# Performance work log

Hardware: AMD Instinct MI355X
Metric: run time of the kernel (lower is better)

## Reference

```python
import jax, jax.numpy as jnp
import numpy as np

N_STREAMS = 4
TAU = 1.0
ALPHA = 0.1
CAYLEY_ITERS = 2
LN_EPS = 1e-5


def setup_inputs() -> dict:
    key = jax.random.key(0)
    k1, k2, k3 = jax.random.split(key, 3)
    b, l, d = 2, 4096, 2048
    n = N_STREAMS
    x = jax.random.normal(k1, (b, l, d), dtype=jnp.float32)
    ln_w = jnp.ones((d,), dtype=jnp.float32)
    ln_b = jnp.zeros((d,), dtype=jnp.float32)
    # CastedLinear: trunc_normal std = 1/sqrt(in_features)
    proj_w = jax.random.truncated_normal(k2, -2.0, 2.0, (3 * n * n, d), dtype=jnp.float32) / jnp.sqrt(d * 1.0)
    proj_b = jnp.zeros((3 * n * n,), dtype=jnp.float32)
    # sublayer_fn realized as a dense linear (typical transformer sublayer core)
    W_sub = jax.random.normal(k3, (d, d), dtype=jnp.float32) / jnp.sqrt(d * 1.0)
    return {"x": x, "ln_w": ln_w, "ln_b": ln_b, "proj_w": proj_w, "proj_b": proj_b, "W_sub": W_sub}


def _layernorm(x, w, b):
    mu = jnp.mean(x, axis=-1, keepdims=True)
    var = jnp.mean(jnp.square(x - mu), axis=-1, keepdims=True)
    return (x - mu) * jax.lax.rsqrt(var + LN_EPS) * w + b


def _iterative_cayley(raw):
    # raw: (b, l, n, n) fp32
    w = raw - jnp.swapaxes(raw, -1, -2)
    eye = jnp.eye(N_STREAMS, dtype=raw.dtype)
    y = eye + ALPHA * w
    for _ in range(CAYLEY_ITERS):
        y = eye + 0.5 * ALPHA * jnp.matmul(w, eye + y)
    return y


def reference(x, ln_w, ln_b, proj_w, proj_b, W_sub):
    b, l, d = x.shape
    n = N_STREAMS
    gates = _layernorm(x, ln_w, ln_b) @ proj_w.T + proj_b  # (b, l, 3*n*n)
    pre_raw, post_raw, res_raw = jnp.split(gates, 3, axis=-1)
    pre_raw = pre_raw.reshape(b, l, n, n).astype(jnp.float32)
    post_raw = post_raw.reshape(b, l, n, n).astype(jnp.float32)
    res_raw = res_raw.reshape(b, l, n, n).astype(jnp.float32)
    h_pre = jax.nn.softmax(pre_raw / TAU, axis=-1)
    h_post = jax.nn.softmax(post_raw / TAU, axis=-2)
    h_res = _iterative_cayley(res_raw)
    # All streams of x_streams are identical copies of x, so
    # einsum('blij,bljd->blid', h, x_streams).mean(-2) == mean_i(sum_j h[i,j]) * x.
    coeff_pre = jnp.mean(jnp.sum(h_pre, axis=-1), axis=-1)    # (b, l)
    coeff_res = jnp.mean(jnp.sum(h_res, axis=-1), axis=-1)    # (b, l)
    coeff_post = jnp.mean(jnp.sum(h_post, axis=-1), axis=-1)  # (b, l)
    x_in = coeff_pre[..., None] * x
    y = x_in @ W_sub  # sublayer_fn
    return coeff_res[..., None] * x + coeff_post[..., None] * y
```

## Files before the change

### kernel.cpp

```cpp
#include <hip/hip_runtime.h>
#include <stdint.h>


typedef __attribute__((ext_vector_type(8))) __bf16 bf16x8;
typedef __attribute__((ext_vector_type(4))) float f32x4;
typedef __attribute__((ext_vector_type(8))) unsigned short us8;
typedef __attribute__((ext_vector_type(4))) unsigned short us4;

__device__ __forceinline__ unsigned short f2bf(float f) {
  union { float f; unsigned int u; } v; v.f = f;
  unsigned int u = v.u;
  u += 0x7fffu + ((u >> 16) & 1u);
  return (unsigned short)(u >> 16);
}

__device__ __forceinline__ void gload_lds16(const void* g, void* l) {
  __builtin_amdgcn_global_load_lds(
      (__attribute__((address_space(1))) void*)g,
      (__attribute__((address_space(3))) void*)l, 16, 0, 0);
}

__global__ __launch_bounds__(256) void k_ln_conv(
    const float* __restrict__ x, const float* __restrict__ lw, const float* __restrict__ lb,
    unsigned short* __restrict__ xb, unsigned short* __restrict__ lnb, int D) {
  const int t = blockIdx.x;
  const int tid = threadIdx.x;
  const float* row = x + (size_t)t * D;
  f32x4 a = *(const f32x4*)(row + tid * 8);
  f32x4 b = *(const f32x4*)(row + tid * 8 + 4);
  float vv[8] = {a[0], a[1], a[2], a[3], b[0], b[1], b[2], b[3]};
  float s = 0.f, ss = 0.f;
#pragma unroll
  for (int j = 0; j < 8; ++j) { s += vv[j]; ss += vv[j] * vv[j]; }
#pragma unroll
  for (int off = 32; off > 0; off >>= 1) { s += __shfl_down(s, off); ss += __shfl_down(ss, off); }
  __shared__ float red[8];
  __shared__ float st[2];
  int lane = tid & 63, wv = tid >> 6;
  if (lane == 0) { red[wv] = s; red[4 + wv] = ss; }
  __syncthreads();
  if (tid == 0) {
    float S = red[0] + red[1] + red[2] + red[3];
    float SS = red[4] + red[5] + red[6] + red[7];
    float mu = S / (float)D;
    float var = SS / (float)D - mu * mu;
    st[0] = mu; st[1] = rsqrtf(var + 1e-5f);
  }
  __syncthreads();
  float mu = st[0], rstd = st[1];
  f32x4 w0 = *(const f32x4*)(lw + tid * 8), w1 = *(const f32x4*)(lw + tid * 8 + 4);
  f32x4 b0 = *(const f32x4*)(lb + tid * 8), b1 = *(const f32x4*)(lb + tid * 8 + 4);
  float ww[8] = {w0[0], w0[1], w0[2], w0[3], w1[0], w1[1], w1[2], w1[3]};
  float bb[8] = {b0[0], b0[1], b0[2], b0[3], b1[0], b1[1], b1[2], b1[3]};
  us8 ox, ol;
#pragma unroll
  for (int j = 0; j < 8; ++j) {
    ox[j] = f2bf(vv[j]);
    ol[j] = f2bf((vv[j] - mu) * rstd * ww[j] + bb[j]);
  }
  *(us8*)(xb + (size_t)t * D + tid * 8) = ox;
  *(us8*)(lnb + (size_t)t * D + tid * 8) = ol;
}

__global__ __launch_bounds__(256) void k_wt(const float* __restrict__ W,
                                            unsigned short* __restrict__ Wt, int D) {
  __shared__ float tile[64][65];
  int kb = blockIdx.x * 64, nb = blockIdx.y * 64;
  int tid = threadIdx.x;
  int tx = tid & 15, ty = tid >> 4;
#pragma unroll
  for (int p = 0; p < 4; ++p) {
    int r = p * 16 + ty;
    f32x4 v = *(const f32x4*)(W + (size_t)(kb + r) * D + nb + tx * 4);
    tile[r][tx * 4 + 0] = v[0]; tile[r][tx * 4 + 1] = v[1];
    tile[r][tx * 4 + 2] = v[2]; tile[r][tx * 4 + 3] = v[3];
  }
  __syncthreads();
#pragma unroll
  for (int p = 0; p < 2; ++p) {
    int c = p * 256 + tid;
    int nr = c >> 3, kc = (c & 7) * 8;
    us8 o;
#pragma unroll
    for (int j = 0; j < 8; ++j) o[j] = f2bf(tile[kc + j][nr]);
    *(us8*)(Wt + (size_t)(nb + nr) * D + kb + kc) = o;
  }
}

__global__ void k_pconv(const float* __restrict__ p, unsigned short* __restrict__ q, int n) {
  int i = (blockIdx.x * 256 + threadIdx.x) * 4;
  if (i < n) {
    f32x4 v = *(const f32x4*)(p + i);
    us4 o;
#pragma unroll
    for (int j = 0; j < 4; ++j) o[j] = f2bf(v[j]);
    *(us4*)(q + i) = o;
  }
}

__global__ __launch_bounds__(256) void k_gates(
    const unsigned short* __restrict__ A,
    const unsigned short* __restrict__ Bp,
    const float* __restrict__ pb,
    float* __restrict__ cresp, float* __restrict__ cpyp, int K) {
  __shared__ __attribute__((aligned(16))) unsigned short As[128 * 32];
  __shared__ __attribute__((aligned(16))) unsigned short Bs[48 * 32];
  __shared__ float gl[128][49];
  __shared__ float pbs[48];
  int tid = threadIdx.x, lane = tid & 63, wv = tid >> 6;
  if (tid < 48) pbs[tid] = pb[tid];
  f32x4 acc[2][3] = {};
  size_t rowBase = (size_t)blockIdx.x * 128;
  for (int k0 = 0; k0 < K; k0 += 32) {
#pragma unroll
    for (int inst = 0; inst < 2; ++inst) {
      int eo = inst * 2048 + wv * 512 + lane * 8;
      int r = eo >> 5, cc = eo & 31;
      gload_lds16(A + (rowBase + r) * K + k0 + cc, (char*)As + inst * 4096 + wv * 1024);
    }
    if (tid < 192) {
      int r = tid >> 2, cc = (tid & 3) * 8;
      us8 v = *(const us8*)(Bp + (size_t)r * K + k0 + cc);
      *(us8*)(Bs + r * 32 + cc) = v;
    }
    __syncthreads();
    int kb = (lane >> 4) * 8, rr = lane & 15;
    bf16x8 av[2], bv[3];
#pragma unroll
    for (int mi = 0; mi < 2; ++mi)
      av[mi] = *(const bf16x8*)(As + (wv * 32 + mi * 16 + rr) * 32 + kb);
#pragma unroll
    for (int ni = 0; ni < 3; ++ni)
      bv[ni] = *(const bf16x8*)(Bs + (ni * 16 + rr) * 32 + kb);
#pragma unroll
    for (int mi = 0; mi < 2; ++mi)
#pragma unroll
      for (int ni = 0; ni < 3; ++ni)
        acc[mi][ni] = __builtin_amdgcn_mfma_f32_16x16x32_bf16(av[mi], bv[ni], acc[mi][ni], 0, 0, 0);
    __syncthreads();
  }
#pragma unroll
  for (int mi = 0; mi < 2; ++mi)
#pragma unroll
    for (int ni = 0; ni < 3; ++ni)
#pragma unroll
      for (int i = 0; i < 4; ++i)
        gl[wv * 32 + mi * 16 + (lane >> 4) * 4 + i][ni * 16 + (lane & 15)] = acc[mi][ni][i];
  __syncthreads();
  if (tid < 128) {
    float g[48];
#pragma unroll
    for (int j = 0; j < 48; ++j) g[j] = gl[tid][j] + pbs[j];
    float cpre = 0.f;
#pragma unroll
    for (int i = 0; i < 4; ++i) {
      float m = fmaxf(fmaxf(g[i * 4], g[i * 4 + 1]), fmaxf(g[i * 4 + 2], g[i * 4 + 3]));
      float e0 = expf(g[i * 4] - m), e1 = expf(g[i * 4 + 1] - m);
      float e2 = expf(g[i * 4 + 2] - m), e3 = expf(g[i * 4 + 3] - m);
      float inv = 1.f / (e0 + e1 + e2 + e3);
      cpre += e0 * inv + e1 * inv + e2 * inv + e3 * inv;
    }
    cpre *= 0.25f;
    float cpost = 0.f;
#pragma unroll
    for (int j = 0; j < 4; ++j) {
      float a0 = g[16 + j], a1 = g[20 + j], a2 = g[24 + j], a3 = g[28 + j];
      float m = fmaxf(fmaxf(a0, a1), fmaxf(a2, a3));
      float e0 = expf(a0 - m), e1 = expf(a1 - m), e2 = expf(a2 - m), e3 = expf(a3 - m);
      float inv = 1.f / (e0 + e1 + e2 + e3);
      cpost += e0 * inv + e1 * inv + e2 * inv + e3 * inv;
    }
    cpost *= 0.25f;
    float w4[16], y4[16];
#pragma unroll
    for (int i = 0; i < 4; ++i)
#pragma unroll
      for (int j = 0; j < 4; ++j)
        w4[i * 4 + j] = g[32 + i * 4 + j] - g[32 + j * 4 + i];
#pragma unroll
    for (int i = 0; i < 16; ++i) y4[i] = 0.1f * w4[i];
    y4[0] += 1.f; y4[5] += 1.f; y4[10] += 1.f; y4[15] += 1.f;
#pragma unroll
    for (int it = 0; it < 2; ++it) {
      float z[16];
#pragma unroll
      for (int i = 0; i < 16; ++i) z[i] = y4[i];
      z[0] += 1.f; z[5] += 1.f; z[10] += 1.f; z[15] += 1.f;
#pragma unroll
      for (int i = 0; i < 4; ++i)
#pragma unroll
        for (int j = 0; j < 4; ++j) {
          float acc2 = 0.f;
#pragma unroll
          for (int k = 0; k < 4; ++k) acc2 += w4[i * 4 + k] * z[k * 4 + j];
          y4[i * 4 + j] = ((i == j) ? 1.f : 0.f) + 0.05f * acc2;
        }
    }
    float cr = 0.f;
#pragma unroll
    for (int i = 0; i < 16; ++i) cr += y4[i];
    cr *= 0.25f;
    cresp[rowBase + tid] = cr;
    cpyp[rowBase + tid] = cpre * cpost;
  }
}

__global__ __launch_bounds__(512, 2) void k_gemm(
    const unsigned short* __restrict__ A,
    const unsigned short* __restrict__ Bt,
    const float* __restrict__ x,
    const float* __restrict__ cresp, const float* __restrict__ cpyp,
    float* __restrict__ out, int M, int N, int K) {
  __shared__ __attribute__((aligned(16))) unsigned short As[2][256 * 64];
  __shared__ __attribute__((aligned(16))) unsigned short Bs[2][256 * 64];
  const int tid = threadIdx.x, lane = tid & 63, wv = tid >> 6;
  const int nbn = N >> 8;
  const int nwg = (M >> 8) * nbn;
  const int chunk = nwg >> 3;
  const int gid = (blockIdx.x & 7) * chunk + (blockIdx.x >> 3);
  const int bm = gid / nbn, bn = gid % nbn;
  const int wm = wv >> 2, wn = wv & 3;
  const int rr = lane & 15, ksl = lane >> 4;
  const int rloc = tid >> 3;
  const int cbelem = (((tid & 7) << 4) ^ ((rloc & 7) << 4)) >> 1;
  const unsigned short* aG = A + (size_t)((bm << 8) + rloc) * K + cbelem;
  const unsigned short* bG = Bt + (size_t)((bn << 8) + rloc) * K + cbelem;
  f32x4 acc[8][4] = {};
  const int nkt = K >> 6;

  auto stage = [&](int kt, int buf) {
    unsigned short* la = &As[buf][wv * 512];
    unsigned short* lb = &Bs[buf][wv * 512];
    const unsigned short* ag = aG + kt * 64;
    const unsigned short* bg = bG + kt * 64;
#pragma unroll
    for (int j = 0; j < 4; ++j) {
      gload_lds16(ag + (size_t)(j << 6) * K, la + j * 4096);
      gload_lds16(bg + (size_t)(j << 6) * K, lb + j * 4096);
    }
  };

  stage(0, 0);
  for (int t = 0; t < nkt; ++t) {
    const int cur = t & 1;
    asm volatile("s_waitcnt vmcnt(0)" ::: "memory");
    __builtin_amdgcn_sched_barrier(0);
    __syncthreads();
    if (t + 1 < nkt) stage(t + 1, cur ^ 1);
    const unsigned short* Ab = &As[cur][(wm * 128) * 64];
    const unsigned short* Bb = &Bs[cur][(wn * 64) * 64];
#pragma unroll
    for (int p = 0; p < 4; ++p) {
      const int kk = p & 1, g = p >> 1;
      const int csw = ((kk * 64 + ksl * 16) ^ ((rr & 7) << 4)) >> 1;
      bf16x8 av[4], bv[4];
#pragma unroll
      for (int m = 0; m < 4; ++m)
        av[m] = *(const bf16x8*)(Ab + ((g * 4 + m) * 16 + rr) * 64 + csw);
#pragma unroll
      for (int n = 0; n < 4; ++n)
        bv[n] = *(const bf16x8*)(Bb + (n * 16 + rr) * 64 + csw);
      __builtin_amdgcn_s_setprio(1);
#pragma unroll
      for (int m = 0; m < 4; ++m)
#pragma unroll
        for (int n = 0; n < 4; ++n)
          acc[g * 4 + m][n] =
              __builtin_amdgcn_mfma_f32_16x16x32_bf16(av[m], bv[n], acc[g * 4 + m][n], 0, 0, 0);
      __builtin_amdgcn_s_setprio(0);
    }
  }

  const int orow0 = (bm << 8) + wm * 128 + ksl * 4;
  const int ocol0 = (bn << 8) + wn * 64 + rr;
#pragma unroll
  for (int mi = 0; mi < 8; ++mi)
#pragma unroll
    for (int i = 0; i < 4; ++i) {
      const int row = orow0 + mi * 16 + i;
      const float crv = cresp[row], cpv = cpyp[row];
      const size_t base = (size_t)row * N + ocol0;
#pragma unroll
      for (int ni = 0; ni < 4; ++ni)
        out[base + ni * 16] = crv * x[base + ni * 16] + cpv * acc[mi][ni][i];
    }
}

extern "C" void kernel_launch(void* const* d_in, const int* in_sizes, int n_in,
                              void* d_out, int out_size, void* d_ws, size_t ws_size,
                              hipStream_t stream) {
  const float* x  = (const float*)d_in[0];
  const float* lw = (const float*)d_in[1];
  const float* lb = (const float*)d_in[2];
  const float* pw = (const float*)d_in[3];
  const float* pb = (const float*)d_in[4];
  const float* W  = (const float*)d_in[5];
  float* out = (float*)d_out;

  const int D = in_sizes[1];
  const int M = in_sizes[0] / D;
  const int G = in_sizes[4];

  char* ws = (char*)d_ws;
  size_t off = 0;
  unsigned short* xb  = (unsigned short*)(ws + off); off += (size_t)M * D * 2;
  unsigned short* lnb = (unsigned short*)(ws + off); off += (size_t)M * D * 2;
  unsigned short* Wt  = (unsigned short*)(ws + off); off += (size_t)D * D * 2;
  unsigned short* pjb = (unsigned short*)(ws + off); off += (size_t)G * D * 2;
  float* cres = (float*)(ws + off); off += (size_t)M * 4;
  float* cpy  = (float*)(ws + off); off += (size_t)M * 4;

  k_ln_conv<<<M, 256, 0, stream>>>(x, lw, lb, xb, lnb, D);
  k_wt<<<dim3(D / 64, D / 64), 256, 0, stream>>>(W, Wt, D);
  k_pconv<<<(G * D / 4 + 255) / 256, 256, 0, stream>>>(pw, pjb, G * D);
  k_gates<<<M / 128, 256, 0, stream>>>(lnb, pjb, pb, cres, cpy, D);

  const int nwg = (M / 256) * (D / 256);
  k_gemm<<<nwg, 512, 0, stream>>>(xb, Wt, x, cres, cpy, out, M, D, D);
}
```

Baseline: 145.9 us.

## Deepen GEMM K-pipeline to a four-slot ring with partial vmcnt waits

The bf16 GEMM main loop moves from a double-buffered 64-wide K tile, which drained every load with vmcnt(0) before each step, to a four-slot LDS ring of 32-wide K slices. Three slices are prefetched ahead, and each step waits only with vmcnt(8) and one s_barrier before issuing the next slice's global-to-LDS loads. The LDS swizzle and fragment addressing are reworked for the narrower tile. The goal is to keep more memory traffic in flight and overlap it with MFMA work, at the cost of more barriers per unit of K and a requirement that the slice count be a multiple of four.

```diff
diff --git a/kernel.cpp b/kernel.cpp
--- a/kernel.cpp
+++ b/kernel.cpp
@@ -211,8 +211,8 @@
     const float* __restrict__ x,
     const float* __restrict__ cresp, const float* __restrict__ cpyp,
     float* __restrict__ out, int M, int N, int K) {
-  __shared__ __attribute__((aligned(16))) unsigned short As[2][256 * 64];
-  __shared__ __attribute__((aligned(16))) unsigned short Bs[2][256 * 64];
+  __shared__ __attribute__((aligned(16))) unsigned short As[4][256 * 32];
+  __shared__ __attribute__((aligned(16))) unsigned short Bs[4][256 * 32];
   const int tid = threadIdx.x, lane = tid & 63, wv = tid >> 6;
   const int nbn = N >> 8;
   const int nwg = (M >> 8) * nbn;
@@ -221,68 +221,79 @@
   const int bm = gid / nbn, bn = gid % nbn;
   const int wm = wv >> 2, wn = wv & 3;
   const int rr = lane & 15, ksl = lane >> 4;
-  const int rloc = tid >> 3;
-  const int cbelem = (((tid & 7) << 4) ^ ((rloc & 7) << 4)) >> 1;
+  const int koff = (ksl ^ ((rr >> 1) & 3)) * 8;
+  const int rloc = tid >> 2;
+  const int cbelem = ((tid & 3) ^ ((tid >> 3) & 3)) * 8;
   const unsigned short* aG = A + (size_t)((bm << 8) + rloc) * K + cbelem;
   const unsigned short* bG = Bt + (size_t)((bn << 8) + rloc) * K + cbelem;
   f32x4 acc[8][4] = {};
-  const int nkt = K >> 6;
-
-  auto stage = [&](int kt, int buf) {
-    unsigned short* la = &As[buf][wv * 512];
-    unsigned short* lb = &Bs[buf][wv * 512];
-    const unsigned short* ag = aG + kt * 64;
-    const unsigned short* bg = bG + kt * 64;
-#pragma unroll
-    for (int j = 0; j < 4; ++j) {
-      gload_lds16(ag + (size_t)(j << 6) * K, la + j * 4096);
-      gload_lds16(bg + (size_t)(j << 6) * K, lb + j * 4096);
-    }
-  };
-
-  stage(0, 0);
-  for (int t = 0; t < nkt; ++t) {
-    const int cur = t & 1;
-    asm volatile("s_waitcnt vmcnt(0)" ::: "memory");
-    __builtin_amdgcn_sched_barrier(0);
-    __syncthreads();
-    if (t + 1 < nkt) stage(t + 1, cur ^ 1);
-    const unsigned short* Ab = &As[cur][(wm * 128) * 64];
-    const unsigned short* Bb = &Bs[cur][(wn * 64) * 64];
-#pragma unroll
-    for (int p = 0; p < 4; ++p) {
-      const int kk = p & 1, g = p >> 1;
-      const int csw = ((kk * 64 + ksl * 16) ^ ((rr & 7) << 4)) >> 1;
-      bf16x8 av[4], bv[4];
-#pragma unroll
-      for (int m = 0; m < 4; ++m)
-        av[m] = *(const bf16x8*)(Ab + ((g * 4 + m) * 16 + rr) * 64 + csw);
-#pragma unroll
-      for (int n = 0; n < 4; ++n)
-        bv[n] = *(const bf16x8*)(Bb + (n * 16 + rr) * 64 + csw);
-      __builtin_amdgcn_s_setprio(1);
-#pragma unroll
-      for (int m = 0; m < 4; ++m)
-#pragma unroll
-        for (int n = 0; n < 4; ++n)
-          acc[g * 4 + m][n] =
-              __builtin_amdgcn_mfma_f32_16x16x32_bf16(av[m], bv[n], acc[g * 4 + m][n], 0, 0, 0);
-      __builtin_amdgcn_s_setprio(0);
-    }
-  }
+  const int nsl = K >> 5;
+
+#define STAGE(KT, SLOT)                                                        \
+  {                                                                            \
+    const unsigned short* ag_ = aG + (KT) * 32;                                \
+    const unsigned short* bg_ = bG + (KT) * 32;                                \
+    unsigned short* la_ = &As[(SLOT)][wv * 512];                               \
+    unsigned short* lb_ = &Bs[(SLOT)][wv * 512];                               \
+    gload_lds16(ag_, la_);                                                     \
+    gload_lds16(ag_ + (size_t)128 * K, la_ + 4096);                            \
+    gload_lds16(bg_, lb_);                                                     \
+    gload_lds16(bg_ + (size_t)128 * K, lb_ + 4096);                            \
+  }
+
+  STAGE(0, 0)
+  STAGE(1, 1)
+  STAGE(2, 2)
+
+#define GBODY(S)                                                               \
+  {                                                                            \
+    asm volatile("s_waitcnt vmcnt(8)" ::: "memory");                           \
+    __builtin_amdgcn_sched_barrier(0);                                         \
+    __builtin_amdgcn_s_barrier();                                              \
+    __builtin_amdgcn_sched_barrier(0);                                         \
+    int kt_ = jb + (S) + 3;                                                    \
+    if (kt_ > nsl - 1) kt_ = nsl - 1;                                          \
+    STAGE(kt_, ((S) + 3) & 3)                                                  \
+    __builtin_amdgcn_sched_barrier(0);                                         \
+    const unsigned short* Ab = &As[(S)][(wm * 128 + rr) * 32 + koff];          \
+    const unsigned short* Bb = &Bs[(S)][(wn * 64 + rr) * 32 + koff];           \
+    bf16x8 av[8], bv[4];                                                       \
+    _Pragma("unroll")                                                          \
+    for (int mf = 0; mf < 8; ++mf) av[mf] = *(const bf16x8*)(Ab + mf * 512);   \
+    _Pragma("unroll")                                                          \
+    for (int nf = 0; nf < 4; ++nf) bv[nf] = *(const bf16x8*)(Bb + nf * 512);   \
+    __builtin_amdgcn_s_setprio(1);                                             \
+    _Pragma("unroll")                                                          \
+    for (int mf = 0; mf < 8; ++mf)                                             \
+      _Pragma("unroll")                                                        \
+      for (int nf = 0; nf < 4; ++nf)                                           \
+        acc[mf][nf] =                                                          \
+            __builtin_amdgcn_mfma_f32_16x16x32_bf16(av[mf], bv[nf],            \
+                                                    acc[mf][nf], 0, 0, 0);     \
+    __builtin_amdgcn_s_setprio(0);                                             \
+  }
+
+  for (int jb = 0; jb < nsl; jb += 4) {
+    GBODY(0)
+    GBODY(1)
+    GBODY(2)
+    GBODY(3)
+  }
+#undef GBODY
+#undef STAGE
 
   const int orow0 = (bm << 8) + wm * 128 + ksl * 4;
   const int ocol0 = (bn << 8) + wn * 64 + rr;
 #pragma unroll
-  for (int mi = 0; mi < 8; ++mi)
+  for (int mf = 0; mf < 8; ++mf)
 #pragma unroll
     for (int i = 0; i < 4; ++i) {
-      const int row = orow0 + mi * 16 + i;
+      const int row = orow0 + mf * 16 + i;
       const float crv = cresp[row], cpv = cpyp[row];
       const size_t base = (size_t)row * N + ocol0;
 #pragma unroll
-      for (int ni = 0; ni < 4; ++ni)
-        out[base + ni * 16] = crv * x[base + ni * 16] + cpv * acc[mi][ni][i];
+      for (int nf = 0; nf < 4; ++nf)
+        out[base + nf * 16] = crv * x[base + nf * 16] + cpv * acc[mf][nf][i];
     }
 }
 
```

After: 139.7 us. 1.04x faster.
